# Kernel tuning notes

Measured on AMD Instinct MI355X. Metric: run time of the kernel, lower is better.

The kernel has to match this reference:

```python
import math
import jax, jax.numpy as jnp
import numpy as np
from jax import lax

NUM_HEADS = 8


def _conv(x, w, b):
    # 3x3 same-padding conv, NCHW / OIHW
    y = lax.conv_general_dilated(x, w, (1, 1), ((1, 1), (1, 1)),
                                 dimension_numbers=("NCHW", "OIHW", "NCHW"))
    return y + b[None, :, None, None]


def setup_inputs() -> dict:
    key = jax.random.key(0)
    ks = jax.random.split(key, 9)
    C = 16
    s = 0.05
    inp = {"x": jax.random.normal(ks[0], (4, C, 256, 512), jnp.float32)}
    names = ["wq", "bq", "wk", "bk", "wv", "bv", "wo", "bo"]
    for i, n in enumerate(names):
        if n.startswith("w"):
            inp[n] = jax.random.normal(ks[i + 1], (C, C, 3, 3), jnp.float32) * s
        else:
            inp[n] = jax.random.normal(ks[i + 1], (C,), jnp.float32) * s
    return inp


def reference(x, wq, bq, wk, bk, wv, bv, wo, bo):
    b, c, h, w = x.shape
    d = h // NUM_HEADS  # per-head feature dim along the height axis

    def split_heads(t):  # (b,c,h,w) -> (b,c,heads,w,d)
        return t.transpose(0, 1, 3, 2).reshape(b, c, w, NUM_HEADS, d).transpose(0, 1, 3, 2, 4)

    q = split_heads(_conv(x, wq, bq)).astype(jnp.float32)
    k = split_heads(_conv(x, wk, bk)).astype(jnp.float32)
    v = split_heads(_conv(x, wv, bv)).astype(jnp.float32)

    # attention over the width (frame) axis, fp32, scaled by sqrt(h)
    qk = jnp.einsum("bcnwd,bcnud->bcnwu", q, k) / math.sqrt(h)
    a = jnp.einsum("bcnwu,bcnud->bcnwd", jax.nn.softmax(qk, axis=-1), v)

    # (b,c,heads,w,d) -> (b,c,w,h) -> (b,c,h,w)
    a = a.transpose(0, 1, 3, 2, 4).reshape(b, c, w, h).transpose(0, 1, 3, 2)
    return _conv(a, wo, bo)
```

## Files before the change

### kernel.cpp

```cpp
#include <hip/hip_runtime.h>

#define BB 4
#define CC 16
#define HH 256
#define WW 512
#define NHD 8
#define DD 32

typedef __attribute__((ext_vector_type(8))) short s8b;
typedef __attribute__((ext_vector_type(4))) float f32x4;
typedef __attribute__((ext_vector_type(4))) unsigned int u32x4;
typedef __attribute__((ext_vector_type(2))) int i32x2;

__device__ inline unsigned cvtpk(float a, float b) {
    unsigned r;
    asm("v_cvt_pk_bf16_f32 %0, %1, %2" : "=v"(r) : "v"(a), "v"(b));
    return r;
}
__device__ inline f32x4 mfma16(u32x4 a, u32x4 b, f32x4 c) {
    return __builtin_amdgcn_mfma_f32_16x16x32_bf16(
        __builtin_bit_cast(s8b, a), __builtin_bit_cast(s8b, b), c, 0, 0, 0);
}

__global__ __launch_bounds__(64)
void wsetup_kernel(const float* __restrict__ w0, const float* __restrict__ w1,
                   const float* __restrict__ w2, const float* __restrict__ w3,
                   unsigned* __restrict__ wfrag)
{
    const int lane = threadIdx.x;
    const int cv = blockIdx.x;
    const float* wg[4] = {w0, w1, w2, w3};
    const int r = lane & 15, g = lane >> 4;
    const int ci0 = (g & 1) * 8;
    #pragma unroll
    for (int kg = 0; kg < 5; ++kg) {
        int tap = 2*kg + (g >> 1);
        unsigned hi[4], lo[4];
        #pragma unroll
        for (int j = 0; j < 4; ++j) {
            float e0 = 0.f, e1 = 0.f;
            if (tap < 9) {
                e0 = wg[cv][(r*CC + ci0 + 2*j    )*9 + tap];
                e1 = wg[cv][(r*CC + ci0 + 2*j + 1)*9 + tap];
            }
            unsigned h = cvtpk(e0, e1);
            float f0 = __builtin_bit_cast(float, h << 16);
            float f1 = __builtin_bit_cast(float, h & 0xffff0000u);
            hi[j] = h;
            lo[j] = cvtpk(e0 - f0, e1 - f1);
        }
        *(u32x4*)(wfrag + (size_t)(((0*4 + cv)*5 + kg)*64 + lane)*4) =
            (u32x4){hi[0], hi[1], hi[2], hi[3]};
        *(u32x4*)(wfrag + (size_t)(((1*4 + cv)*5 + kg)*64 + lane)*4) =
            (u32x4){lo[0], lo[1], lo[2], lo[3]};
    }
}

__global__ __launch_bounds__(256)
void xpack_kernel(const float* __restrict__ x, unsigned* __restrict__ xcl)
{
    __shared__ float xsf[8][16][68];
    const int tid = threadIdx.x;
    const int bx = blockIdx.x, by = blockIdx.y, bz = blockIdx.z;
    const float* xb = x + (size_t)bz*CC*HH*WW + (size_t)(by*8)*WW + bx*64;

    #pragma unroll
    for (int k = 0; k < 8; ++k) {
        int idx = tid + k*256;
        int ci  = idx >> 7;
        int rem = idx & 127;
        int hh  = rem >> 4;
        int qq  = rem & 15;
        f32x4 v = *(const f32x4*)(xb + (size_t)ci*HH*WW + (size_t)hh*WW + qq*4);
        *(f32x4*)&xsf[hh][ci][qq*4] = v;
    }
    __syncthreads();

    #pragma unroll
    for (int k = 0; k < 2; ++k) {
        int p  = tid + k*256;
        int hh = p >> 6, ww = p & 63;
        unsigned pk[8];
        #pragma unroll
        for (int q = 0; q < 8; ++q)
            pk[q] = cvtpk(xsf[hh][2*q][ww], xsf[hh][2*q+1][ww]);
        unsigned* op = xcl + ((size_t)(bz*HH + by*8 + hh)*WW + bx*64 + ww)*8;
        *(u32x4*)(op    ) = (u32x4){pk[0], pk[1], pk[2], pk[3]};
        *(u32x4*)(op + 4) = (u32x4){pk[4], pk[5], pk[6], pk[7]};
    }
}

template<int NC, int CVB, int INMODE, bool OUT_PAIRED, int NTERM>
__global__ __launch_bounds__(256)
void conv_mfma_kernel(const void* __restrict__ xin,
                      const unsigned* __restrict__ wfrag,
                      const float* __restrict__ b0, const float* __restrict__ b1,
                      const float* __restrict__ b2,
                      unsigned* __restrict__ o0, unsigned* __restrict__ o1,
                      unsigned* __restrict__ o2, float* __restrict__ of,
                      float kscale)
{
    constexpr int LC2 = 34, NPX = 18*34;
    constexpr int PXB = (NTERM == 3) ? 64 : 32;
    __shared__ __align__(16) unsigned char xs[NPX*PXB];

    const int tid = threadIdx.x;
    const int bx = blockIdx.x, by = blockIdx.y, bz = blockIdx.z;
    const int lane = tid & 63, wid = tid >> 6;
    const int g = lane >> 4, r = lane & 15;

    u32x4 wh[NC][5], wl[NC][5];
    #pragma unroll
    for (int cv = 0; cv < NC; ++cv)
        #pragma unroll
        for (int kg = 0; kg < 5; ++kg) {
            wh[cv][kg] = *(const u32x4*)(wfrag + (size_t)(((CVB+cv)*5 + kg)*64 + lane)*4);
            if constexpr (NTERM >= 2)
                wl[cv][kg] = *(const u32x4*)(wfrag + (size_t)(((4+CVB+cv)*5 + kg)*64 + lane)*4);
        }
    const float* bg[3] = {b0, b1, b2};
    f32x4 bias[NC];
    #pragma unroll
    for (int cv = 0; cv < NC; ++cv) bias[cv] = *(const f32x4*)(bg[cv] + 4*g);

    const int row0 = by*16 - 1, col0 = bx*32 - 1;
    for (int idx = tid; idx < NPX; idx += 256) {
        int rr = idx / LC2, cc2 = idx - rr*LC2;
        int gr = row0 + rr, gc = col0 + cc2;
        bool ok = (gr >= 0) & (gr < HH) & (gc >= 0) & (gc < WW);
        if constexpr (INMODE == 2) {
            const unsigned* xb = (const unsigned*)xin + (size_t)bz*HH*WW*8;
            int grc = gr < 0 ? 0 : (gr > HH-1 ? HH-1 : gr);
            int gcc = gc < 0 ? 0 : (gc > WW-1 ? WW-1 : gc);
            const unsigned* px = xb + ((size_t)grc*WW + gcc)*8;
            u32x4 A = *(const u32x4*)(px);
            u32x4 Bv = *(const u32x4*)(px + 4);
            if (!ok) { A = (u32x4){0,0,0,0}; Bv = (u32x4){0,0,0,0}; }
            unsigned base = (unsigned)idx*32, m = ((unsigned)idx & 4) << 2;
            *(u32x4*)(xs + base + (( 0u) ^ m)) = A;
            *(u32x4*)(xs + base + ((16u) ^ m)) = Bv;
            continue;
        }
        unsigned hi[8];
        if constexpr (INMODE == 1) {
            const unsigned* xb = (const unsigned*)xin + (size_t)bz*CC*(HH/2)*WW;
            int grc = gr < 0 ? 0 : (gr > HH-1 ? HH-1 : gr);
            int gcc = gc < 0 ? 0 : (gc > WW-1 ? WW-1 : gc);
            const unsigned* px = xb + (size_t)(grc >> 1)*WW + gcc;
            unsigned wv[16];
            #pragma unroll
            for (int c8 = 0; c8 < 16; ++c8)
                wv[c8] = ok ? px[(size_t)c8*(HH/2)*WW] : 0u;
            const unsigned sel = (grc & 1) ? 0x07060302u : 0x05040100u;
            #pragma unroll
            for (int p = 0; p < 8; ++p)
                hi[p] = __builtin_amdgcn_perm(wv[2*p+1], wv[2*p], sel);
        } else if constexpr (INMODE == 0) {
            const float* xb = (const float*)xin + (size_t)bz*CC*HH*WW;
            const float* px = xb + (size_t)gr*WW + gc;
            float v0[16];
            #pragma unroll
            for (int c8 = 0; c8 < 16; ++c8) v0[c8] = ok ? px[(size_t)c8*HH*WW] : 0.f;
            #pragma unroll
            for (int p = 0; p < 8; ++p) hi[p] = cvtpk(v0[2*p], v0[2*p+1]);
            if constexpr (NTERM == 3) {
                unsigned lo[8];
                #pragma unroll
                for (int p = 0; p < 8; ++p) {
                    float f0 = __builtin_bit_cast(float, hi[p] << 16);
                    float f1 = __builtin_bit_cast(float, hi[p] & 0xffff0000u);
                    lo[p] = cvtpk(v0[2*p] - f0, v0[2*p+1] - f1);
                }
                unsigned base = (unsigned)idx*64, m = ((unsigned)idx & 3) << 4;
                *(u32x4*)(xs + base + ((32u) ^ m)) = (u32x4){lo[0], lo[1], lo[2], lo[3]};
                *(u32x4*)(xs + base + ((48u) ^ m)) = (u32x4){lo[4], lo[5], lo[6], lo[7]};
            }
        }
        if constexpr (NTERM == 3) {
            unsigned base = (unsigned)idx*64, m = ((unsigned)idx & 3) << 4;
            *(u32x4*)(xs + base + (( 0u) ^ m)) = (u32x4){hi[0], hi[1], hi[2], hi[3]};
            *(u32x4*)(xs + base + ((16u) ^ m)) = (u32x4){hi[4], hi[5], hi[6], hi[7]};
        } else {
            unsigned base = (unsigned)idx*32, m = ((unsigned)idx & 4) << 2;
            *(u32x4*)(xs + base + (( 0u) ^ m)) = (u32x4){hi[0], hi[1], hi[2], hi[3]};
            *(u32x4*)(xs + base + ((16u) ^ m)) = (u32x4){hi[4], hi[5], hi[6], hi[7]};
        }
    }
    __syncthreads();

    int pk_base[5];
    #pragma unroll
    for (int kg = 0; kg < 5; ++kg) {
        int tap = 2*kg + (g >> 1);
        if (tap > 8) tap = 8;
        pk_base[kg] = (tap/3)*LC2 + (tap%3) + r;
    }
    const unsigned sh = (unsigned)(g & 1) << 4;

    auto tile = [&](int hr, int wt, f32x4* acc) {
        const int tb = hr*LC2 + wt*16;
        #pragma unroll
        for (int kg = 0; kg < 5; ++kg) {
            int px = tb + pk_base[kg];
            if constexpr (NTERM == 3) {
                unsigned b_ = (unsigned)px*64, m = ((unsigned)px & 3) << 4;
                u32x4 Bh = *(const u32x4*)(xs + b_ + ( sh        ^ m));
                u32x4 Bl = *(const u32x4*)(xs + b_ + ((sh | 32u) ^ m));
                #pragma unroll
                for (int cv = 0; cv < NC; ++cv) {
                    acc[cv] = mfma16(wh[cv][kg], Bh, acc[cv]);
                    acc[cv] = mfma16(wl[cv][kg], Bh, acc[cv]);
                    acc[cv] = mfma16(wh[cv][kg], Bl, acc[cv]);
                }
            } else {
                unsigned b_ = (unsigned)px*32, m = ((unsigned)px & 4) << 2;
                u32x4 Bh = *(const u32x4*)(xs + b_ + (sh ^ m));
                #pragma unroll
                for (int cv = 0; cv < NC; ++cv) {
                    acc[cv] = mfma16(wh[cv][kg], Bh, acc[cv]);
                    if constexpr (NTERM >= 2)
                        acc[cv] = mfma16(wl[cv][kg], Bh, acc[cv]);
                }
            }
        }
    };

    #pragma unroll 1
    for (int hp = 0; hp < 2; ++hp) {
        const int hrE = 4*wid + 2*hp;
        #pragma unroll 1
        for (int wt = 0; wt < 2; ++wt) {
            const int col = bx*32 + wt*16 + r;
            if constexpr (OUT_PAIRED) {
                f32x4 aE[NC];
                #pragma unroll
                for (int cv = 0; cv < NC; ++cv) aE[cv] = (f32x4){0.f,0.f,0.f,0.f};
                tile(hrE, wt, aE);
                unsigned Ep[NC][2];
                #pragma unroll
                for (int cv = 0; cv < NC; ++cv) {
                    const float sc = (cv == 1) ? kscale : 1.0f;
                    Ep[cv][0] = cvtpk((aE[cv][0] + bias[cv][0])*sc, (aE[cv][1] + bias[cv][1])*sc);
                    Ep[cv][1] = cvtpk((aE[cv][2] + bias[cv][2])*sc, (aE[cv][3] + bias[cv][3])*sc);
                }
                f32x4 aO[NC];
                #pragma unroll
                for (int cv = 0; cv < NC; ++cv) aO[cv] = (f32x4){0.f,0.f,0.f,0.f};
                tile(hrE + 1, wt, aO);
                const int hpix = by*8 + 2*wid + hp;
                #pragma unroll
                for (int cv = 0; cv < NC; ++cv) {
                    const float sc = (cv == 1) ? kscale : 1.0f;
                    unsigned Op0 = cvtpk((aO[cv][0] + bias[cv][0])*sc, (aO[cv][1] + bias[cv][1])*sc);
                    unsigned Op1 = cvtpk((aO[cv][2] + bias[cv][2])*sc, (aO[cv][3] + bias[cv][3])*sc);
                    unsigned wd[4] = {
                        __builtin_amdgcn_perm(Op0, Ep[cv][0], 0x05040100u),
                        __builtin_amdgcn_perm(Op0, Ep[cv][0], 0x07060302u),
                        __builtin_amdgcn_perm(Op1, Ep[cv][1], 0x05040100u),
                        __builtin_amdgcn_perm(Op1, Ep[cv][1], 0x07060302u) };
                    unsigned* op = (cv == 0) ? o0 : (cv == 1) ? o1 : o2;
                    #pragma unroll
                    for (int reg = 0; reg < 4; ++reg)
                        op[((size_t)(bz*CC + 4*g + reg)*(HH/2) + hpix)*WW + col] = wd[reg];
                }
            } else {
                #pragma unroll 1
                for (int e = 0; e < 2; ++e) {
                    f32x4 a0[1] = {(f32x4){0.f,0.f,0.f,0.f}};
                    tile(hrE + e, wt, a0);
                    const int h = by*16 + hrE + e;
                    #pragma unroll
                    for (int reg = 0; reg < 4; ++reg)
                        of[((size_t)(bz*CC + 4*g + reg)*HH + h)*WW + col] =
                            a0[0][reg] + bias[0][reg];
                }
            }
        }
    }
}

__global__ __launch_bounds__(512)
void attn_mfma_kernel(const unsigned* __restrict__ q,
                      const unsigned* __restrict__ k,
                      const unsigned* __restrict__ v,
                      unsigned* __restrict__ apk)
{
    __shared__ __align__(16) unsigned char Kl[WW*DD*2];
    __shared__ __align__(16) unsigned char Vl[DD*WW*2];

    const int s  = blockIdx.x;
    const int n  = s & (NHD-1);
    const int bc = s >> 3;
    const int pbase = (bc*(HH/2) + n*(DD/2)) * WW;
    const unsigned* qg = q + pbase;
    const unsigned* kg = k + pbase;
    const unsigned* vg = v + pbase;
    unsigned* ag = apk + pbase;

    const int tid = threadIdx.x;

    {
        const int key = tid;
        unsigned pk[16];
        #pragma unroll
        for (int dp = 0; dp < 16; ++dp) pk[dp] = kg[(size_t)dp*WW + key];
        #pragma unroll
        for (int j = 0; j < 4; ++j) {
            unsigned off = (unsigned)(key*64 + j*16) ^ ((unsigned)(key&7) << 4);
            *(u32x4*)(Kl + off) = (u32x4){pk[4*j], pk[4*j+1], pk[4*j+2], pk[4*j+3]};
        }
    }
    {
        const int dp = tid >> 5;
        const int k0 = (tid & 31) * 16;
        unsigned rowE[8], rowO[8];
        #pragma unroll
        for (int j = 0; j < 4; ++j) {
            u32x4 U = *(const u32x4*)(vg + (size_t)dp*WW + k0 + 4*j);
            rowE[2*j  ] = __builtin_amdgcn_perm(U[1], U[0], 0x05040100u);
            rowE[2*j+1] = __builtin_amdgcn_perm(U[3], U[2], 0x05040100u);
            rowO[2*j  ] = __builtin_amdgcn_perm(U[1], U[0], 0x07060302u);
            rowO[2*j+1] = __builtin_amdgcn_perm(U[3], U[2], 0x07060302u);
        }
        const int d0 = 2*dp, d1 = 2*dp + 1;
        const unsigned bE = (unsigned)(d0*1024 + k0*2);
        const unsigned bO = (unsigned)(d1*1024 + k0*2);
        const unsigned mE = ((unsigned)d0 & 7u) << 4;
        const unsigned mO = ((unsigned)d1 & 7u) << 4;
        *(u32x4*)(Vl + ((bE     ) ^ mE)) = (u32x4){rowE[0], rowE[1], rowE[4], rowE[5]};
        *(u32x4*)(Vl + ((bE + 16) ^ mE)) = (u32x4){rowE[2], rowE[3], rowE[6], rowE[7]};
        *(u32x4*)(Vl + ((bO     ) ^ mO)) = (u32x4){rowO[0], rowO[1], rowO[4], rowO[5]};
        *(u32x4*)(Vl + ((bO + 16) ^ mO)) = (u32x4){rowO[2], rowO[3], rowO[6], rowO[7]};
    }

    const int wid  = tid >> 6;
    const int lane = tid & 63;
    const int g = lane >> 4;
    const int r = lane & 15;
    const int w0 = wid * 64;

    u32x4 qf[4];
    #pragma unroll
    for (int rf = 0; rf < 4; ++rf) {
        const int row = w0 + rf*16 + r;
        unsigned pq[4];
        #pragma unroll
        for (int jj = 0; jj < 4; ++jj)
            pq[jj] = qg[(size_t)(4*g + jj)*WW + row];
        qf[rf] = (u32x4){pq[0], pq[1], pq[2], pq[3]};
    }

    __syncthreads();

    const u32x4 vones = (r == 0)
        ? (u32x4){0x3F803F80u, 0x3F803F80u, 0x3F803F80u, 0x3F803F80u}
        : (u32x4){0u, 0u, 0u, 0u};

    f32x4 oacc[4][2];
    f32x4 lacc[4];
    #pragma unroll
    for (int qi = 0; qi < 4; ++qi) {
        oacc[qi][0] = (f32x4){0.f,0.f,0.f,0.f};
        oacc[qi][1] = (f32x4){0.f,0.f,0.f,0.f};
        lacc[qi]    = (f32x4){0.f,0.f,0.f,0.f};
    }

    #pragma unroll 1
    for (int j0 = 0; j0 < WW; j0 += 32) {
        u32x4 kf[2];
        #pragma unroll
        for (int cf = 0; cf < 2; ++cf) {
            const int key = j0 + cf*16 + r;
            unsigned off = (unsigned)(key*64 + g*16) ^ ((unsigned)(key&7) << 4);
            kf[cf] = *(const u32x4*)(Kl + off);
        }
        u32x4 vf[2];
        #pragma unroll
        for (int cfd = 0; cfd < 2; ++cfd) {
            const int d = r + 16*cfd;
            unsigned off = (unsigned)(d*1024 + (j0 + 8*g)*2) ^ ((unsigned)(d&7) << 4);
            vf[cfd] = *(const u32x4*)(Vl + off);
        }

        f32x4 sacc[4][2];
        #pragma unroll
        for (int qi = 0; qi < 4; ++qi) {
            sacc[qi][0] = mfma16(kf[0], qf[qi], (f32x4){0.f,0.f,0.f,0.f});
            sacc[qi][1] = mfma16(kf[1], qf[qi], (f32x4){0.f,0.f,0.f,0.f});
        }

        #pragma unroll
        for (int qi = 0; qi < 4; ++qi) {
            float p0 = __builtin_amdgcn_exp2f(sacc[qi][0][0]);
            float p1 = __builtin_amdgcn_exp2f(sacc[qi][0][1]);
            float p2 = __builtin_amdgcn_exp2f(sacc[qi][0][2]);
            float p3 = __builtin_amdgcn_exp2f(sacc[qi][0][3]);
            float p4 = __builtin_amdgcn_exp2f(sacc[qi][1][0]);
            float p5 = __builtin_amdgcn_exp2f(sacc[qi][1][1]);
            float p6 = __builtin_amdgcn_exp2f(sacc[qi][1][2]);
            float p7 = __builtin_amdgcn_exp2f(sacc[qi][1][3]);
            unsigned Aw = cvtpk(p0, p1);
            unsigned Bw = cvtpk(p2, p3);
            unsigned Cw = cvtpk(p4, p5);
            unsigned Dw = cvtpk(p6, p7);
            i32x2 w02 = __builtin_amdgcn_permlane32_swap((int)Aw, (int)Cw, false, false);
            i32x2 w13 = __builtin_amdgcn_permlane32_swap((int)Bw, (int)Dw, false, false);
            u32x4 pa = (u32x4){ (unsigned)w02[0], (unsigned)w13[0],
                                (unsigned)w02[1], (unsigned)w13[1] };
            oacc[qi][0] = mfma16(vf[0], pa, oacc[qi][0]);
            oacc[qi][1] = mfma16(vf[1], pa, oacc[qi][1]);
            lacc[qi]    = mfma16(vones, pa, lacc[qi]);
        }
    }

    #pragma unroll
    for (int qi = 0; qi < 4; ++qi) {
        float l = __shfl(lacc[qi][0], r);
        float inv = 1.0f / l;
        const int qcol = w0 + qi*16 + r;
        #pragma unroll
        for (int cfd = 0; cfd < 2; ++cfd) {
            const int dpair = 8*cfd + 2*g;
            unsigned P0 = cvtpk(oacc[qi][cfd][0]*inv, oacc[qi][cfd][1]*inv);
            unsigned P1 = cvtpk(oacc[qi][cfd][2]*inv, oacc[qi][cfd][3]*inv);
            ag[(size_t)(dpair    )*WW + qcol] = P0;
            ag[(size_t)(dpair + 1)*WW + qcol] = P1;
        }
    }
}

extern "C" void kernel_launch(void* const* d_in, const int* in_sizes, int n_in,
                              void* d_out, int out_size, void* d_ws, size_t ws_size,
                              hipStream_t stream) {
    (void)in_sizes; (void)n_in; (void)out_size; (void)ws_size;
    const float* x  = (const float*)d_in[0];
    const float* wq = (const float*)d_in[1];
    const float* bq = (const float*)d_in[2];
    const float* wk = (const float*)d_in[3];
    const float* bk = (const float*)d_in[4];
    const float* wv = (const float*)d_in[5];
    const float* bv = (const float*)d_in[6];
    const float* wo = (const float*)d_in[7];
    const float* bo = (const float*)d_in[8];
    float* out = (float*)d_out;

    const float SC = 0.0625f * 1.44269504088896340736f;

    const size_t S = (size_t)BB*CC*HH*WW;
    unsigned* apk  = (unsigned*)d_ws;
    unsigned* qpk  = apk + S/2;
    unsigned* kpk  = qpk + S/2;
    unsigned* vpk  = kpk + S/2;
    unsigned* xcl  = vpk + S/2;
    unsigned* wfrag = xcl + S/2;

    wsetup_kernel<<<dim3(4), 64, 0, stream>>>(wq, wk, wv, wo, wfrag);
    xpack_kernel<<<dim3(WW/64, HH/8, BB), 256, 0, stream>>>(x, xcl);
    dim3 cgrid(WW/32, HH/16, BB);
    conv_mfma_kernel<3, 0, 2, true, 1><<<cgrid, 256, 0, stream>>>(
        xcl, wfrag, bq, bk, bv, qpk, kpk, vpk, nullptr, SC);
    attn_mfma_kernel<<<dim3(512), 512, 0, stream>>>(qpk, kpk, vpk, apk);
    conv_mfma_kernel<1, 3, 1, false, 2><<<cgrid, 256, 0, stream>>>(
        apk, wfrag, bo, bo, bo, nullptr, nullptr, nullptr, out, 1.0f);
}
```

Baseline: 77.15 us.

## Split attention K/V staging into two chunks to overlap loads with compute

The attention kernel now stages K and V into LDS in two 256-key chunks. The second chunk's global loads are issued before the first chunk's compute, so their latency can overlap with the MFMA work. The conv kernel also drops its unused fp32-input/three-term path and always uses the 32-byte-per-pixel layout. The pipelining adds registers to hold the staged chunk and a second barrier.

```diff
diff --git a/kernel.cpp b/kernel.cpp
--- a/kernel.cpp
+++ b/kernel.cpp
@@ -10,6 +10,7 @@
 typedef __attribute__((ext_vector_type(8))) short s8b;
 typedef __attribute__((ext_vector_type(4))) float f32x4;
 typedef __attribute__((ext_vector_type(4))) unsigned int u32x4;
+typedef __attribute__((ext_vector_type(2))) unsigned int u32x2;
 typedef __attribute__((ext_vector_type(2))) int i32x2;
 
 __device__ inline unsigned cvtpk(float a, float b) {
@@ -101,8 +102,7 @@
                       float kscale)
 {
     constexpr int LC2 = 34, NPX = 18*34;
-    constexpr int PXB = (NTERM == 3) ? 64 : 32;
-    __shared__ __align__(16) unsigned char xs[NPX*PXB];
+    __shared__ __align__(16) unsigned char xs[NPX*32];
 
     const int tid = threadIdx.x;
     const int bx = blockIdx.x, by = blockIdx.y, bz = blockIdx.z;
@@ -139,10 +139,7 @@
             unsigned base = (unsigned)idx*32, m = ((unsigned)idx & 4) << 2;
             *(u32x4*)(xs + base + (( 0u) ^ m)) = A;
             *(u32x4*)(xs + base + ((16u) ^ m)) = Bv;
-            continue;
-        }
-        unsigned hi[8];
-        if constexpr (INMODE == 1) {
+        } else {
             const unsigned* xb = (const unsigned*)xin + (size_t)bz*CC*(HH/2)*WW;
             int grc = gr < 0 ? 0 : (gr > HH-1 ? HH-1 : gr);
             int gcc = gc < 0 ? 0 : (gc > WW-1 ? WW-1 : gc);
@@ -152,35 +149,10 @@
             for (int c8 = 0; c8 < 16; ++c8)
                 wv[c8] = ok ? px[(size_t)c8*(HH/2)*WW] : 0u;
             const unsigned sel = (grc & 1) ? 0x07060302u : 0x05040100u;
+            unsigned hi[8];
             #pragma unroll
             for (int p = 0; p < 8; ++p)
                 hi[p] = __builtin_amdgcn_perm(wv[2*p+1], wv[2*p], sel);
-        } else if constexpr (INMODE == 0) {
-            const float* xb = (const float*)xin + (size_t)bz*CC*HH*WW;
-            const float* px = xb + (size_t)gr*WW + gc;
-            float v0[16];
-            #pragma unroll
-            for (int c8 = 0; c8 < 16; ++c8) v0[c8] = ok ? px[(size_t)c8*HH*WW] : 0.f;
-            #pragma unroll
-            for (int p = 0; p < 8; ++p) hi[p] = cvtpk(v0[2*p], v0[2*p+1]);
-            if constexpr (NTERM == 3) {
-                unsigned lo[8];
-                #pragma unroll
-                for (int p = 0; p < 8; ++p) {
-                    float f0 = __builtin_bit_cast(float, hi[p] << 16);
-                    float f1 = __builtin_bit_cast(float, hi[p] & 0xffff0000u);
-                    lo[p] = cvtpk(v0[2*p] - f0, v0[2*p+1] - f1);
-                }
-                unsigned base = (unsigned)idx*64, m = ((unsigned)idx & 3) << 4;
-                *(u32x4*)(xs + base + ((32u) ^ m)) = (u32x4){lo[0], lo[1], lo[2], lo[3]};
-                *(u32x4*)(xs + base + ((48u) ^ m)) = (u32x4){lo[4], lo[5], lo[6], lo[7]};
-            }
-        }
-        if constexpr (NTERM == 3) {
-            unsigned base = (unsigned)idx*64, m = ((unsigned)idx & 3) << 4;
-            *(u32x4*)(xs + base + (( 0u) ^ m)) = (u32x4){hi[0], hi[1], hi[2], hi[3]};
-            *(u32x4*)(xs + base + ((16u) ^ m)) = (u32x4){hi[4], hi[5], hi[6], hi[7]};
-        } else {
             unsigned base = (unsigned)idx*32, m = ((unsigned)idx & 4) << 2;
             *(u32x4*)(xs + base + (( 0u) ^ m)) = (u32x4){hi[0], hi[1], hi[2], hi[3]};
             *(u32x4*)(xs + base + ((16u) ^ m)) = (u32x4){hi[4], hi[5], hi[6], hi[7]};
@@ -202,25 +174,13 @@
         #pragma unroll
         for (int kg = 0; kg < 5; ++kg) {
             int px = tb + pk_base[kg];
-            if constexpr (NTERM == 3) {
-                unsigned b_ = (unsigned)px*64, m = ((unsigned)px & 3) << 4;
-                u32x4 Bh = *(const u32x4*)(xs + b_ + ( sh        ^ m));
-                u32x4 Bl = *(const u32x4*)(xs + b_ + ((sh | 32u) ^ m));
-                #pragma unroll
-                for (int cv = 0; cv < NC; ++cv) {
-                    acc[cv] = mfma16(wh[cv][kg], Bh, acc[cv]);
+            unsigned b_ = (unsigned)px*32, m = ((unsigned)px & 4) << 2;
+            u32x4 Bh = *(const u32x4*)(xs + b_ + (sh ^ m));
+            #pragma unroll
+            for (int cv = 0; cv < NC; ++cv) {
+                acc[cv] = mfma16(wh[cv][kg], Bh, acc[cv]);
+                if constexpr (NTERM >= 2)
                     acc[cv] = mfma16(wl[cv][kg], Bh, acc[cv]);
-                    acc[cv] = mfma16(wh[cv][kg], Bl, acc[cv]);
-                }
-            } else {
-                unsigned b_ = (unsigned)px*32, m = ((unsigned)px & 4) << 2;
-                u32x4 Bh = *(const u32x4*)(xs + b_ + (sh ^ m));
-                #pragma unroll
-                for (int cv = 0; cv < NC; ++cv) {
-                    acc[cv] = mfma16(wh[cv][kg], Bh, acc[cv]);
-                    if constexpr (NTERM >= 2)
-                        acc[cv] = mfma16(wl[cv][kg], Bh, acc[cv]);
-                }
             }
         }
     };
@@ -285,8 +245,8 @@
                       const unsigned* __restrict__ v,
                       unsigned* __restrict__ apk)
 {
-    __shared__ __align__(16) unsigned char Kl[WW*DD*2];
-    __shared__ __align__(16) unsigned char Vl[DD*WW*2];
+    __shared__ __align__(16) unsigned char Kc[2][16384];
+    __shared__ __align__(16) unsigned char Vc[2][16384];
 
     const int s  = blockIdx.x;
     const int n  = s & (NHD-1);
@@ -298,46 +258,53 @@
     unsigned* ag = apk + pbase;
 
     const int tid = threadIdx.x;
-
-    {
-        const int key = tid;
-        unsigned pk[16];
-        #pragma unroll
-        for (int dp = 0; dp < 16; ++dp) pk[dp] = kg[(size_t)dp*WW + key];
-        #pragma unroll
-        for (int j = 0; j < 4; ++j) {
-            unsigned off = (unsigned)(key*64 + j*16) ^ ((unsigned)(key&7) << 4);
-            *(u32x4*)(Kl + off) = (u32x4){pk[4*j], pk[4*j+1], pk[4*j+2], pk[4*j+3]};
-        }
-    }
-    {
-        const int dp = tid >> 5;
-        const int k0 = (tid & 31) * 16;
-        unsigned rowE[8], rowO[8];
-        #pragma unroll
-        for (int j = 0; j < 4; ++j) {
-            u32x4 U = *(const u32x4*)(vg + (size_t)dp*WW + k0 + 4*j);
-            rowE[2*j  ] = __builtin_amdgcn_perm(U[1], U[0], 0x05040100u);
-            rowE[2*j+1] = __builtin_amdgcn_perm(U[3], U[2], 0x05040100u);
-            rowO[2*j  ] = __builtin_amdgcn_perm(U[1], U[0], 0x07060302u);
-            rowO[2*j+1] = __builtin_amdgcn_perm(U[3], U[2], 0x07060302u);
-        }
-        const int d0 = 2*dp, d1 = 2*dp + 1;
-        const unsigned bE = (unsigned)(d0*1024 + k0*2);
-        const unsigned bO = (unsigned)(d1*1024 + k0*2);
-        const unsigned mE = ((unsigned)d0 & 7u) << 4;
-        const unsigned mO = ((unsigned)d1 & 7u) << 4;
-        *(u32x4*)(Vl + ((bE     ) ^ mE)) = (u32x4){rowE[0], rowE[1], rowE[4], rowE[5]};
-        *(u32x4*)(Vl + ((bE + 16) ^ mE)) = (u32x4){rowE[2], rowE[3], rowE[6], rowE[7]};
-        *(u32x4*)(Vl + ((bO     ) ^ mO)) = (u32x4){rowO[0], rowO[1], rowO[4], rowO[5]};
-        *(u32x4*)(Vl + ((bO + 16) ^ mO)) = (u32x4){rowO[2], rowO[3], rowO[6], rowO[7]};
-    }
-
-    const int wid  = tid >> 6;
-    const int lane = tid & 63;
-    const int g = lane >> 4;
-    const int r = lane & 15;
+    const int wid = tid >> 6, lane = tid & 63;
+    const int g = lane >> 4, r = lane & 15;
     const int w0 = wid * 64;
+
+    const int kl = tid & 255, jh = tid >> 8;
+    const unsigned ksw = ((unsigned)kl & 7u) << 4;
+    const int vdp = tid >> 5, vt = tid & 31;
+    const int vk0 = vt * 8;
+    const int vgix = vt >> 1, vodd = vt & 1;
+    const int vd0 = 2*vdp, vd1 = vd0 + 1;
+    const unsigned vbase0 = (unsigned)(vd0*512 + vgix*32 + vodd*8);
+    const unsigned vbase1 = (unsigned)(vd1*512 + vgix*32 + vodd*8);
+    const unsigned vsw0 = ((unsigned)vd0 & 7u) << 4;
+    const unsigned vsw1 = ((unsigned)vd1 & 7u) << 4;
+
+    unsigned kst[8];
+    u32x4 vst0, vst1;
+
+    auto stage_load = [&](int c) {
+        const int cb = c*256;
+        #pragma unroll
+        for (int i = 0; i < 8; ++i)
+            kst[i] = kg[(size_t)(8*jh + i)*WW + cb + kl];
+        const unsigned* vr = vg + (size_t)vdp*WW + cb + vk0;
+        vst0 = *(const u32x4*)(vr);
+        vst1 = *(const u32x4*)(vr + 4);
+    };
+    auto stage_write = [&](int b) {
+        *(u32x4*)(Kc[b] + (((unsigned)(kl*64 + jh*32     )) ^ ksw)) =
+            (u32x4){kst[0], kst[1], kst[2], kst[3]};
+        *(u32x4*)(Kc[b] + (((unsigned)(kl*64 + jh*32 + 16)) ^ ksw)) =
+            (u32x4){kst[4], kst[5], kst[6], kst[7]};
+        unsigned E0 = __builtin_amdgcn_perm(vst0[1], vst0[0], 0x05040100u);
+        unsigned E1 = __builtin_amdgcn_perm(vst0[3], vst0[2], 0x05040100u);
+        unsigned E2 = __builtin_amdgcn_perm(vst1[1], vst1[0], 0x05040100u);
+        unsigned E3 = __builtin_amdgcn_perm(vst1[3], vst1[2], 0x05040100u);
+        unsigned O0 = __builtin_amdgcn_perm(vst0[1], vst0[0], 0x07060302u);
+        unsigned O1 = __builtin_amdgcn_perm(vst0[3], vst0[2], 0x07060302u);
+        unsigned O2 = __builtin_amdgcn_perm(vst1[1], vst1[0], 0x07060302u);
+        unsigned O3 = __builtin_amdgcn_perm(vst1[3], vst1[2], 0x07060302u);
+        *(u32x2*)(Vc[b] + ((vbase0       ) ^ vsw0)) = (u32x2){E0, E1};
+        *(u32x2*)(Vc[b] + ((vbase0 + 16u) ^ vsw0)) = (u32x2){E2, E3};
+        *(u32x2*)(Vc[b] + ((vbase1       ) ^ vsw1)) = (u32x2){O0, O1};
+        *(u32x2*)(Vc[b] + ((vbase1 + 16u) ^ vsw1)) = (u32x2){O2, O3};
+    };
+
+    stage_load(0);
 
     u32x4 qf[4];
     #pragma unroll
@@ -350,6 +317,7 @@
         qf[rf] = (u32x4){pq[0], pq[1], pq[2], pq[3]};
     }
 
+    stage_write(0);
     __syncthreads();
 
     const u32x4 vones = (r == 0)
@@ -366,51 +334,57 @@
     }
 
     #pragma unroll 1
-    for (int j0 = 0; j0 < WW; j0 += 32) {
-        u32x4 kf[2];
-        #pragma unroll
-        for (int cf = 0; cf < 2; ++cf) {
-            const int key = j0 + cf*16 + r;
-            unsigned off = (unsigned)(key*64 + g*16) ^ ((unsigned)(key&7) << 4);
-            kf[cf] = *(const u32x4*)(Kl + off);
-        }
-        u32x4 vf[2];
-        #pragma unroll
-        for (int cfd = 0; cfd < 2; ++cfd) {
-            const int d = r + 16*cfd;
-            unsigned off = (unsigned)(d*1024 + (j0 + 8*g)*2) ^ ((unsigned)(d&7) << 4);
-            vf[cfd] = *(const u32x4*)(Vl + off);
-        }
-
-        f32x4 sacc[4][2];
-        #pragma unroll
-        for (int qi = 0; qi < 4; ++qi) {
-            sacc[qi][0] = mfma16(kf[0], qf[qi], (f32x4){0.f,0.f,0.f,0.f});
-            sacc[qi][1] = mfma16(kf[1], qf[qi], (f32x4){0.f,0.f,0.f,0.f});
-        }
-
-        #pragma unroll
-        for (int qi = 0; qi < 4; ++qi) {
-            float p0 = __builtin_amdgcn_exp2f(sacc[qi][0][0]);
-            float p1 = __builtin_amdgcn_exp2f(sacc[qi][0][1]);
-            float p2 = __builtin_amdgcn_exp2f(sacc[qi][0][2]);
-            float p3 = __builtin_amdgcn_exp2f(sacc[qi][0][3]);
-            float p4 = __builtin_amdgcn_exp2f(sacc[qi][1][0]);
-            float p5 = __builtin_amdgcn_exp2f(sacc[qi][1][1]);
-            float p6 = __builtin_amdgcn_exp2f(sacc[qi][1][2]);
-            float p7 = __builtin_amdgcn_exp2f(sacc[qi][1][3]);
-            unsigned Aw = cvtpk(p0, p1);
-            unsigned Bw = cvtpk(p2, p3);
-            unsigned Cw = cvtpk(p4, p5);
-            unsigned Dw = cvtpk(p6, p7);
-            i32x2 w02 = __builtin_amdgcn_permlane32_swap((int)Aw, (int)Cw, false, false);
-            i32x2 w13 = __builtin_amdgcn_permlane32_swap((int)Bw, (int)Dw, false, false);
-            u32x4 pa = (u32x4){ (unsigned)w02[0], (unsigned)w13[0],
-                                (unsigned)w02[1], (unsigned)w13[1] };
-            oacc[qi][0] = mfma16(vf[0], pa, oacc[qi][0]);
-            oacc[qi][1] = mfma16(vf[1], pa, oacc[qi][1]);
-            lacc[qi]    = mfma16(vones, pa, lacc[qi]);
-        }
+    for (int c = 0; c < 2; ++c) {
+        if (c == 0) stage_load(1);
+        #pragma unroll 1
+        for (int jt = 0; jt < 8; ++jt) {
+            const int j0l = jt*32;
+            u32x4 kf[2];
+            #pragma unroll
+            for (int cf = 0; cf < 2; ++cf) {
+                const int key = j0l + cf*16 + r;
+                unsigned off = ((unsigned)(key*64 + g*16)) ^ (((unsigned)key & 7u) << 4);
+                kf[cf] = *(const u32x4*)(Kc[c] + off);
+            }
+            u32x4 vf[2];
+            #pragma unroll
+            for (int cfd = 0; cfd < 2; ++cfd) {
+                const int d = r + 16*cfd;
+                unsigned off = ((unsigned)(d*512 + (j0l + 8*g)*2)) ^ (((unsigned)d & 7u) << 4);
+                vf[cfd] = *(const u32x4*)(Vc[c] + off);
+            }
+
+            f32x4 sacc[4][2];
+            #pragma unroll
+            for (int qi = 0; qi < 4; ++qi) {
+                sacc[qi][0] = mfma16(kf[0], qf[qi], (f32x4){0.f,0.f,0.f,0.f});
+                sacc[qi][1] = mfma16(kf[1], qf[qi], (f32x4){0.f,0.f,0.f,0.f});
+            }
+
+            #pragma unroll
+            for (int qi = 0; qi < 4; ++qi) {
+                float p0 = __builtin_amdgcn_exp2f(sacc[qi][0][0]);
+                float p1 = __builtin_amdgcn_exp2f(sacc[qi][0][1]);
+                float p2 = __builtin_amdgcn_exp2f(sacc[qi][0][2]);
+                float p3 = __builtin_amdgcn_exp2f(sacc[qi][0][3]);
+                float p4 = __builtin_amdgcn_exp2f(sacc[qi][1][0]);
+                float p5 = __builtin_amdgcn_exp2f(sacc[qi][1][1]);
+                float p6 = __builtin_amdgcn_exp2f(sacc[qi][1][2]);
+                float p7 = __builtin_amdgcn_exp2f(sacc[qi][1][3]);
+                unsigned Aw = cvtpk(p0, p1);
+                unsigned Bw = cvtpk(p2, p3);
+                unsigned Cw = cvtpk(p4, p5);
+                unsigned Dw = cvtpk(p6, p7);
+                i32x2 w02 = __builtin_amdgcn_permlane32_swap((int)Aw, (int)Cw, false, false);
+                i32x2 w13 = __builtin_amdgcn_permlane32_swap((int)Bw, (int)Dw, false, false);
+                u32x4 pa = (u32x4){ (unsigned)w02[0], (unsigned)w13[0],
+                                    (unsigned)w02[1], (unsigned)w13[1] };
+                oacc[qi][0] = mfma16(vf[0], pa, oacc[qi][0]);
+                oacc[qi][1] = mfma16(vf[1], pa, oacc[qi][1]);
+                lacc[qi]    = mfma16(vones, pa, lacc[qi]);
+            }
+        }
+        if (c == 0) { stage_write(1); __syncthreads(); }
     }
 
     #pragma unroll
```

After: 77.89 us. About the same (+1.0%).

## Fuse weight setup into xpack and stage output-conv input via LDS

Applied to the files above, without the earlier changes.

The weight-fragment setup kernel becomes an extra z-slice of the xpack grid, which removes one kernel launch. The output conv (INMODE 1) now loads its raw packed input tile into shared memory with coalesced loads first, then builds the per-pixel channel fragments from LDS instead of doing 16 strided global loads per pixel. Unused NTERM==3 and INMODE==0 paths are removed. The cost is extra LDS (about 21KB), which may lower occupancy, plus an additional barrier.

```diff
diff --git a/kernel.cpp b/kernel.cpp
--- a/kernel.cpp
+++ b/kernel.cpp
@@ -22,46 +22,48 @@
         __builtin_bit_cast(s8b, a), __builtin_bit_cast(s8b, b), c, 0, 0, 0);
 }
 
-__global__ __launch_bounds__(64)
-void wsetup_kernel(const float* __restrict__ w0, const float* __restrict__ w1,
-                   const float* __restrict__ w2, const float* __restrict__ w3,
-                   unsigned* __restrict__ wfrag)
-{
-    const int lane = threadIdx.x;
-    const int cv = blockIdx.x;
-    const float* wg[4] = {w0, w1, w2, w3};
-    const int r = lane & 15, g = lane >> 4;
-    const int ci0 = (g & 1) * 8;
-    #pragma unroll
-    for (int kg = 0; kg < 5; ++kg) {
-        int tap = 2*kg + (g >> 1);
-        unsigned hi[4], lo[4];
-        #pragma unroll
-        for (int j = 0; j < 4; ++j) {
-            float e0 = 0.f, e1 = 0.f;
-            if (tap < 9) {
-                e0 = wg[cv][(r*CC + ci0 + 2*j    )*9 + tap];
-                e1 = wg[cv][(r*CC + ci0 + 2*j + 1)*9 + tap];
-            }
-            unsigned h = cvtpk(e0, e1);
-            float f0 = __builtin_bit_cast(float, h << 16);
-            float f1 = __builtin_bit_cast(float, h & 0xffff0000u);
-            hi[j] = h;
-            lo[j] = cvtpk(e0 - f0, e1 - f1);
-        }
-        *(u32x4*)(wfrag + (size_t)(((0*4 + cv)*5 + kg)*64 + lane)*4) =
-            (u32x4){hi[0], hi[1], hi[2], hi[3]};
-        *(u32x4*)(wfrag + (size_t)(((1*4 + cv)*5 + kg)*64 + lane)*4) =
-            (u32x4){lo[0], lo[1], lo[2], lo[3]};
-    }
-}
-
 __global__ __launch_bounds__(256)
-void xpack_kernel(const float* __restrict__ x, unsigned* __restrict__ xcl)
+void xpack_kernel(const float* __restrict__ x, unsigned* __restrict__ xcl,
+                  const float* __restrict__ w0, const float* __restrict__ w1,
+                  const float* __restrict__ w2, const float* __restrict__ w3,
+                  unsigned* __restrict__ wfrag)
 {
     __shared__ float xsf[8][16][68];
     const int tid = threadIdx.x;
     const int bx = blockIdx.x, by = blockIdx.y, bz = blockIdx.z;
+
+    if (bz == BB) {
+        if (bx >= 4 || by != 0 || tid >= 64) return;
+        const int lane = tid;
+        const int cv = bx;
+        const float* wg[4] = {w0, w1, w2, w3};
+        const int r = lane & 15, g = lane >> 4;
+        const int ci0 = (g & 1) * 8;
+        #pragma unroll
+        for (int kg = 0; kg < 5; ++kg) {
+            int tap = 2*kg + (g >> 1);
+            unsigned hi[4], lo[4];
+            #pragma unroll
+            for (int j = 0; j < 4; ++j) {
+                float e0 = 0.f, e1 = 0.f;
+                if (tap < 9) {
+                    e0 = wg[cv][(r*CC + ci0 + 2*j    )*9 + tap];
+                    e1 = wg[cv][(r*CC + ci0 + 2*j + 1)*9 + tap];
+                }
+                unsigned h = cvtpk(e0, e1);
+                float f0 = __builtin_bit_cast(float, h << 16);
+                float f1 = __builtin_bit_cast(float, h & 0xffff0000u);
+                hi[j] = h;
+                lo[j] = cvtpk(e0 - f0, e1 - f1);
+            }
+            *(u32x4*)(wfrag + (size_t)(((0*4 + cv)*5 + kg)*64 + lane)*4) =
+                (u32x4){hi[0], hi[1], hi[2], hi[3]};
+            *(u32x4*)(wfrag + (size_t)(((1*4 + cv)*5 + kg)*64 + lane)*4) =
+                (u32x4){lo[0], lo[1], lo[2], lo[3]};
+        }
+        return;
+    }
+
     const float* xb = x + (size_t)bz*CC*HH*WW + (size_t)(by*8)*WW + bx*64;
 
     #pragma unroll
@@ -101,8 +103,8 @@
                       float kscale)
 {
     constexpr int LC2 = 34, NPX = 18*34;
-    constexpr int PXB = (NTERM == 3) ? 64 : 32;
-    __shared__ __align__(16) unsigned char xs[NPX*PXB];
+    __shared__ __align__(16) unsigned char xs[NPX*32];
+    __shared__ unsigned rawv[(INMODE == 1) ? 16*10*34 : 1];
 
     const int tid = threadIdx.x;
     const int bx = blockIdx.x, by = blockIdx.y, bz = blockIdx.z;
@@ -124,11 +126,44 @@
     for (int cv = 0; cv < NC; ++cv) bias[cv] = *(const f32x4*)(bg[cv] + 4*g);
 
     const int row0 = by*16 - 1, col0 = bx*32 - 1;
-    for (int idx = tid; idx < NPX; idx += 256) {
-        int rr = idx / LC2, cc2 = idx - rr*LC2;
-        int gr = row0 + rr, gc = col0 + cc2;
-        bool ok = (gr >= 0) & (gr < HH) & (gc >= 0) & (gc < WW);
-        if constexpr (INMODE == 2) {
+
+    if constexpr (INMODE == 1) {
+        const unsigned* xb = (const unsigned*)xin + (size_t)bz*CC*(HH/2)*WW;
+        const int hpbase = 8*by - 1;
+        for (int idx = tid; idx < 16*10*34; idx += 256) {
+            int c   = idx / 340;
+            int rem = idx - c*340;
+            int hpr = rem / 34;
+            int wr  = rem - hpr*34;
+            int hpg = hpbase + hpr; hpg = hpg < 0 ? 0 : (hpg > 127 ? 127 : hpg);
+            int gcc = col0 + wr;    gcc = gcc < 0 ? 0 : (gcc > WW-1 ? WW-1 : gcc);
+            rawv[idx] = xb[(size_t)c*(HH/2)*WW + (size_t)hpg*WW + gcc];
+        }
+        __syncthreads();
+        for (int idx = tid; idx < NPX; idx += 256) {
+            int rr = idx / LC2, cc2 = idx - rr*LC2;
+            int gr = row0 + rr;
+            bool ok = (gr >= 0) & (gr < HH) & ((col0 + cc2) >= 0) & ((col0 + cc2) < WW);
+            int grc = gr < 0 ? 0 : (gr > HH-1 ? HH-1 : gr);
+            int hl  = (grc >> 1) - hpbase;
+            const unsigned sel = (grc & 1) ? 0x07060302u : 0x05040100u;
+            unsigned wv[16];
+            #pragma unroll
+            for (int c8 = 0; c8 < 16; ++c8)
+                wv[c8] = ok ? rawv[c8*340 + hl*34 + cc2] : 0u;
+            unsigned hi[8];
+            #pragma unroll
+            for (int p = 0; p < 8; ++p)
+                hi[p] = __builtin_amdgcn_perm(wv[2*p+1], wv[2*p], sel);
+            unsigned base = (unsigned)idx*32, m = ((unsigned)idx & 4) << 2;
+            *(u32x4*)(xs + base + (( 0u) ^ m)) = (u32x4){hi[0], hi[1], hi[2], hi[3]};
+            *(u32x4*)(xs + base + ((16u) ^ m)) = (u32x4){hi[4], hi[5], hi[6], hi[7]};
+        }
+    } else {
+        for (int idx = tid; idx < NPX; idx += 256) {
+            int rr = idx / LC2, cc2 = idx - rr*LC2;
+            int gr = row0 + rr, gc = col0 + cc2;
+            bool ok = (gr >= 0) & (gr < HH) & (gc >= 0) & (gc < WW);
             const unsigned* xb = (const unsigned*)xin + (size_t)bz*HH*WW*8;
             int grc = gr < 0 ? 0 : (gr > HH-1 ? HH-1 : gr);
             int gcc = gc < 0 ? 0 : (gc > WW-1 ? WW-1 : gc);
@@ -139,51 +174,6 @@
             unsigned base = (unsigned)idx*32, m = ((unsigned)idx & 4) << 2;
             *(u32x4*)(xs + base + (( 0u) ^ m)) = A;
             *(u32x4*)(xs + base + ((16u) ^ m)) = Bv;
-            continue;
-        }
-        unsigned hi[8];
-        if constexpr (INMODE == 1) {
-            const unsigned* xb = (const unsigned*)xin + (size_t)bz*CC*(HH/2)*WW;
-            int grc = gr < 0 ? 0 : (gr > HH-1 ? HH-1 : gr);
-            int gcc = gc < 0 ? 0 : (gc > WW-1 ? WW-1 : gc);
-            const unsigned* px = xb + (size_t)(grc >> 1)*WW + gcc;
-            unsigned wv[16];
-            #pragma unroll
-            for (int c8 = 0; c8 < 16; ++c8)
-                wv[c8] = ok ? px[(size_t)c8*(HH/2)*WW] : 0u;
-            const unsigned sel = (grc & 1) ? 0x07060302u : 0x05040100u;
-            #pragma unroll
-            for (int p = 0; p < 8; ++p)
-                hi[p] = __builtin_amdgcn_perm(wv[2*p+1], wv[2*p], sel);
-        } else if constexpr (INMODE == 0) {
-            const float* xb = (const float*)xin + (size_t)bz*CC*HH*WW;
-            const float* px = xb + (size_t)gr*WW + gc;
-            float v0[16];
-            #pragma unroll
-            for (int c8 = 0; c8 < 16; ++c8) v0[c8] = ok ? px[(size_t)c8*HH*WW] : 0.f;
-            #pragma unroll
-            for (int p = 0; p < 8; ++p) hi[p] = cvtpk(v0[2*p], v0[2*p+1]);
-            if constexpr (NTERM == 3) {
-                unsigned lo[8];
-                #pragma unroll
-                for (int p = 0; p < 8; ++p) {
-                    float f0 = __builtin_bit_cast(float, hi[p] << 16);
-                    float f1 = __builtin_bit_cast(float, hi[p] & 0xffff0000u);
-                    lo[p] = cvtpk(v0[2*p] - f0, v0[2*p+1] - f1);
-                }
-                unsigned base = (unsigned)idx*64, m = ((unsigned)idx & 3) << 4;
-                *(u32x4*)(xs + base + ((32u) ^ m)) = (u32x4){lo[0], lo[1], lo[2], lo[3]};
-                *(u32x4*)(xs + base + ((48u) ^ m)) = (u32x4){lo[4], lo[5], lo[6], lo[7]};
-            }
-        }
-        if constexpr (NTERM == 3) {
-            unsigned base = (unsigned)idx*64, m = ((unsigned)idx & 3) << 4;
-            *(u32x4*)(xs + base + (( 0u) ^ m)) = (u32x4){hi[0], hi[1], hi[2], hi[3]};
-            *(u32x4*)(xs + base + ((16u) ^ m)) = (u32x4){hi[4], hi[5], hi[6], hi[7]};
-        } else {
-            unsigned base = (unsigned)idx*32, m = ((unsigned)idx & 4) << 2;
-            *(u32x4*)(xs + base + (( 0u) ^ m)) = (u32x4){hi[0], hi[1], hi[2], hi[3]};
-            *(u32x4*)(xs + base + ((16u) ^ m)) = (u32x4){hi[4], hi[5], hi[6], hi[7]};
         }
     }
     __syncthreads();
@@ -202,25 +192,13 @@
         #pragma unroll
         for (int kg = 0; kg < 5; ++kg) {
             int px = tb + pk_base[kg];
-            if constexpr (NTERM == 3) {
-                unsigned b_ = (unsigned)px*64, m = ((unsigned)px & 3) << 4;
-                u32x4 Bh = *(const u32x4*)(xs + b_ + ( sh        ^ m));
-                u32x4 Bl = *(const u32x4*)(xs + b_ + ((sh | 32u) ^ m));
-                #pragma unroll
-                for (int cv = 0; cv < NC; ++cv) {
-                    acc[cv] = mfma16(wh[cv][kg], Bh, acc[cv]);
+            unsigned b_ = (unsigned)px*32, m = ((unsigned)px & 4) << 2;
+            u32x4 Bh = *(const u32x4*)(xs + b_ + (sh ^ m));
+            #pragma unroll
+            for (int cv = 0; cv < NC; ++cv) {
+                acc[cv] = mfma16(wh[cv][kg], Bh, acc[cv]);
+                if constexpr (NTERM >= 2)
                     acc[cv] = mfma16(wl[cv][kg], Bh, acc[cv]);
-                    acc[cv] = mfma16(wh[cv][kg], Bl, acc[cv]);
-                }
-            } else {
-                unsigned b_ = (unsigned)px*32, m = ((unsigned)px & 4) << 2;
-                u32x4 Bh = *(const u32x4*)(xs + b_ + (sh ^ m));
-                #pragma unroll
-                for (int cv = 0; cv < NC; ++cv) {
-                    acc[cv] = mfma16(wh[cv][kg], Bh, acc[cv]);
-                    if constexpr (NTERM >= 2)
-                        acc[cv] = mfma16(wl[cv][kg], Bh, acc[cv]);
-                }
             }
         }
     };
@@ -454,8 +432,8 @@
     unsigned* xcl  = vpk + S/2;
     unsigned* wfrag = xcl + S/2;
 
-    wsetup_kernel<<<dim3(4), 64, 0, stream>>>(wq, wk, wv, wo, wfrag);
-    xpack_kernel<<<dim3(WW/64, HH/8, BB), 256, 0, stream>>>(x, xcl);
+    xpack_kernel<<<dim3(WW/64, HH/8, BB+1), 256, 0, stream>>>(
+        x, xcl, wq, wk, wv, wo, wfrag);
     dim3 cgrid(WW/32, HH/16, BB);
     conv_mfma_kernel<3, 0, 2, true, 1><<<cgrid, 256, 0, stream>>>(
         xcl, wfrag, bq, bk, bv, qpk, kpk, vpk, nullptr, SC);
```

After: 74.93 us, median of 3. 1.03x faster.
